# Performance work log

Measured on AMD Instinct MI355X. Metric: run time of the kernel, lower is better.

Reference implementation:

```python
import jax, jax.numpy as jnp
import numpy as np

N = 100000  # number of nodes
SELF_LOOP_W = 2.0  # improved=True in PyG GCNConv


def gcn_conv(x, edge_index, W, b):
    # x: [N, Fin], edge_index: [2, E] (row=src, col=dst), W: [Fin, Fout], b: [Fout]
    src, dst = edge_index[0], edge_index[1]
    h = x @ W  # [N, Fout]
    # degree with improved self-loops (weight 2.0)
    ones = jnp.ones(src.shape, dtype=h.dtype)
    deg = jax.ops.segment_sum(ones, dst, num_segments=N) + SELF_LOOP_W
    dinv = jnp.where(deg > 0, jax.lax.rsqrt(deg), 0.0)
    norm = dinv[src] * dinv[dst]  # [E]
    agg = jax.ops.segment_sum(h[src] * norm[:, None], dst, num_segments=N)
    # self-loop contribution: weight 2.0, norm = dinv_i * 2 * dinv_i
    agg = agg + h * (SELF_LOOP_W * dinv * dinv)[:, None]
    return agg + b


def setup_inputs() -> dict:
    key = jax.random.key(0)
    ks = jax.random.split(key, 6)
    x = jax.random.normal(ks[0], (N, 64), dtype=jnp.float32)
    edge_index = jax.random.randint(ks[1], (2, 1600000), 0, N, dtype=jnp.int64)
    W1 = jax.random.normal(ks[2], (64, 64), dtype=jnp.float32) * 0.1
    b1 = jax.random.normal(ks[3], (64,), dtype=jnp.float32) * 0.1
    W2 = jax.random.normal(ks[4], (64, 32), dtype=jnp.float32) * 0.1
    b2 = jax.random.normal(ks[5], (32,), dtype=jnp.float32) * 0.1
    return {"x": x, "edge_index": edge_index, "W1": W1, "b1": b1, "W2": W2, "b2": b2}


def reference(x, edge_index, W1, b1, W2, b2):
    h1 = jax.nn.relu(gcn_conv(x, edge_index, W1, b1))
    feature_map = h1
    out = gcn_conv(h1, edge_index, W2, b2)
    return (out, feature_map)
```

## Files before the change

kernel.cpp:

```cpp
#include <hip/hip_runtime.h>

#define N_NODES 100000
#define E_EDGES 1600000

#define BSHIFT 7
#define BSIZE 128
#define NBUCK ((N_NODES + BSIZE - 1) / BSIZE)
#define STAGE_TPB 1024
#define STAGE_EPT 16
#define STAGE_CHUNK (STAGE_TPB * STAGE_EPT)
#define NREP 4
#define BUCKET_CAP 4096

typedef __attribute__((ext_vector_type(8))) short short8;
typedef __attribute__((ext_vector_type(4))) float float4v;

__device__ inline unsigned short f2bf(float f) {
    union { float f; unsigned u; } t; t.f = f;
    unsigned r = (t.u + 0x7fffu + ((t.u >> 16) & 1u)) >> 16;
    return (unsigned short)r;
}
__device__ inline float bf2f(unsigned short h) {
    union { unsigned u; float f; } t; t.u = ((unsigned)h) << 16; return t.f;
}
__device__ inline unsigned pack_bf16x2(float a, float b) {
    return (unsigned)f2bf(a) | ((unsigned)f2bf(b) << 16);
}
__device__ inline float bf_lo(unsigned u) { union { unsigned u; float f; } t; t.u = u << 16; return t.f; }
__device__ inline float bf_hi(unsigned u) { union { unsigned u; float f; } t; t.u = u & 0xffff0000u; return t.f; }

__global__ void cursor_init_kernel(int* __restrict__ gcursor) {
    int b = blockIdx.x * blockDim.x + threadIdx.x;
    if (b < NBUCK) gcursor[b] = b * BUCKET_CAP;
}

__global__ void __launch_bounds__(STAGE_TPB) stage_kernel(
    const int* __restrict__ src, const int* __restrict__ dst,
    int* __restrict__ gcursor, unsigned* __restrict__ staged, int E) {
    __shared__ int hist[NREP][NBUCK];
    __shared__ int base[NREP][NBUCK];
    const int tid = threadIdx.x;
    const int rep = (tid >> 8) & (NREP - 1);
    const int e0 = blockIdx.x * STAGE_CHUNK;
    for (int i = tid; i < NREP * NBUCK; i += STAGE_TPB) ((int*)hist)[i] = 0;
    __syncthreads();
    int d[STAGE_EPT], s[STAGE_EPT];
#pragma unroll
    for (int k = 0; k < STAGE_EPT; ++k) {
        int e = e0 + k * STAGE_TPB + tid;
        if (e < E) {
            d[k] = dst[e];
            s[k] = src[e];
            atomicAdd(&hist[rep][d[k] >> BSHIFT], 1);
        } else {
            d[k] = -1;
        }
    }
    __syncthreads();
    for (int i = tid; i < NBUCK; i += STAGE_TPB) {
        int h0 = hist[0][i], h1 = hist[1][i], h2 = hist[2][i], h3 = hist[3][i];
        int t = h0 + h1 + h2 + h3;
        if (t > 0) {
            int g = atomicAdd(&gcursor[i], t);
            base[0][i] = g;
            base[1][i] = g + h0;
            base[2][i] = g + h0 + h1;
            base[3][i] = g + h0 + h1 + h2;
        }
    }
    __syncthreads();
#pragma unroll
    for (int k = 0; k < STAGE_EPT; ++k) {
        if (d[k] >= 0) {
            int b = d[k] >> BSHIFT;
            int pos = atomicAdd(&base[rep][b], 1);
            if (pos < (b + 1) * BUCKET_CAP)
                staged[pos] = (unsigned)s[k] | ((unsigned)(d[k] & (BSIZE - 1)) << 17);
        }
    }
}

__global__ void bscan_kernel(const int* __restrict__ gcursor, int* __restrict__ boff) {
    __shared__ int s[1024];
    const int tid = threadIdx.x;
    int v = 0;
    if (tid < NBUCK) {
        v = gcursor[tid] - tid * BUCKET_CAP;
        if (v > BUCKET_CAP) v = BUCKET_CAP;
    }
    s[tid] = v;
    __syncthreads();
    for (int off = 1; off < 1024; off <<= 1) {
        int t = (tid >= off) ? s[tid - off] : 0;
        __syncthreads();
        s[tid] += t;
        __syncthreads();
    }
    if (tid < NBUCK) boff[tid] = s[tid] - v;
    if (tid == NBUCK - 1) boff[NBUCK] = s[tid];
}

__global__ void bucket_csr_kernel(const unsigned* __restrict__ staged,
                                  const int* __restrict__ boff,
                                  int* __restrict__ deg, float* __restrict__ dinv,
                                  int* __restrict__ rowptr, int* __restrict__ csrc, int n) {
    __shared__ int ldeg[BSIZE];
    __shared__ int lrp[BSIZE];
    __shared__ int lcnt[BSIZE];
    __shared__ unsigned lrec[BUCKET_CAP];
    __shared__ int lsrc[BUCKET_CAP];
    const int b = blockIdx.x;
    const int node0 = b * BSIZE;
    const int nn = min(BSIZE, n - node0);
    const int tid = threadIdx.x;
    if (tid < BSIZE) { ldeg[tid] = 0; lcnt[tid] = 0; }
    __syncthreads();
    const int ebase = boff[b];
    const int ecnt = min(boff[b + 1] - ebase, BUCKET_CAP);
    const int sbase = b * BUCKET_CAP;
    for (int i = tid; i < ecnt; i += 256) {
        unsigned r = staged[sbase + i];
        lrec[i] = r;
        atomicAdd(&ldeg[r >> 17], 1);
    }
    __syncthreads();
    int mydeg = (tid < BSIZE) ? ldeg[tid] : 0;
    if (tid < BSIZE) lrp[tid] = mydeg;
    __syncthreads();
    for (int off = 1; off < BSIZE; off <<= 1) {
        int v = 0;
        if (tid < BSIZE && tid >= off) v = lrp[tid - off];
        __syncthreads();
        if (tid < BSIZE) lrp[tid] += v;
        __syncthreads();
    }
    if (tid < BSIZE) {
        int ex = lrp[tid] - mydeg;
        lrp[tid] = ex;
        if (tid < nn) {
            deg[node0 + tid] = mydeg;
            dinv[node0 + tid] = rsqrtf((float)mydeg + 2.0f);
            rowptr[node0 + tid] = ebase + ex;
        }
    }
    __syncthreads();
    for (int i = tid; i < ecnt; i += 256) {
        unsigned r = lrec[i];
        int dl = (int)(r >> 17);
        int sv = (int)(r & 0x1FFFFu);
        int pos = lrp[dl] + atomicAdd(&lcnt[dl], 1);
        if (pos < BUCKET_CAP) lsrc[pos] = sv;
    }
    __syncthreads();
    for (int i = tid; i < ecnt; i += 256)
        csrc[ebase + i] = lsrc[i];
}

template <int FOUT>
__global__ void __launch_bounds__(256) linear_mfma_kernel(
    const float* __restrict__ X, const float* __restrict__ W,
    const float* __restrict__ dinv, unsigned* __restrict__ HS, int n) {
    constexpr int NT = FOUT / 16;
    const int NTILES_M = n / 16;
    const int lane = threadIdx.x & 63;
    const int gwave = blockIdx.x * 4 + (threadIdx.x >> 6);
    const int nwaves = gridDim.x * 4;
    const int m = lane & 15;
    const int q = lane >> 4;

    short8 Bhi[2][NT], Blo[2][NT];
#pragma unroll
    for (int ks = 0; ks < 2; ++ks)
#pragma unroll
        for (int nt = 0; nt < NT; ++nt) {
            short8 bh, bl;
#pragma unroll
            for (int j = 0; j < 8; ++j) {
                int k = ks * 32 + q * 8 + j;
                float wv = W[k * FOUT + nt * 16 + m];
                unsigned short h = f2bf(wv);
                bh[j] = (short)h;
                bl[j] = (short)f2bf(wv - bf2f(h));
            }
            Bhi[ks][nt] = bh;
            Blo[ks][nt] = bl;
        }

    for (int tile = gwave; tile < NTILES_M; tile += nwaves) {
        const int row0 = tile * 16;
        float4v C[NT];
#pragma unroll
        for (int nt = 0; nt < NT; ++nt) C[nt] = (float4v){0.f, 0.f, 0.f, 0.f};
#pragma unroll
        for (int ks = 0; ks < 2; ++ks) {
            const float* xp = X + (size_t)(row0 + m) * 64 + ks * 32 + q * 8;
            float4v x0 = *(const float4v*)xp;
            float4v x1 = *(const float4v*)(xp + 4);
            short8 Ahi, Alo;
#pragma unroll
            for (int j = 0; j < 4; ++j) {
                unsigned short h0 = f2bf(x0[j]);
                Ahi[j] = (short)h0;
                Alo[j] = (short)f2bf(x0[j] - bf2f(h0));
                unsigned short h1 = f2bf(x1[j]);
                Ahi[4 + j] = (short)h1;
                Alo[4 + j] = (short)f2bf(x1[j] - bf2f(h1));
            }
#pragma unroll
            for (int nt = 0; nt < NT; ++nt) {
                C[nt] = __builtin_amdgcn_mfma_f32_16x16x32_bf16(Ahi, Bhi[ks][nt], C[nt], 0, 0, 0);
                C[nt] = __builtin_amdgcn_mfma_f32_16x16x32_bf16(Alo, Bhi[ks][nt], C[nt], 0, 0, 0);
                C[nt] = __builtin_amdgcn_mfma_f32_16x16x32_bf16(Ahi, Blo[ks][nt], C[nt], 0, 0, 0);
            }
        }
#pragma unroll
        for (int ch = 0; ch < NT / 2; ++ch) {
#pragma unroll
            for (int reg = 0; reg < 4; ++reg) {
                int r = row0 + q * 4 + reg;
                float di = dinv[r];
                unsigned u = pack_bf16x2(C[2 * ch][reg] * di, C[2 * ch + 1][reg] * di);
                HS[(size_t)ch * n * 16 + (size_t)r * 16 + m] = u;
            }
        }
    }
}

template <bool RELU>
__global__ void gather_chunk_kernel(const int* __restrict__ rowptr, const int* __restrict__ deg,
                                    const int* __restrict__ csrc, const unsigned* __restrict__ HS,
                                    const float* __restrict__ dinv, const float* __restrict__ bias0,
                                    float* __restrict__ OUT, int out_stride, int out_off,
                                    int n) {
    constexpr int G = 16;
    constexpr int NPB = 256 / G;
    int node = blockIdx.x * NPB + (threadIdx.x / G);
    int l = threadIdx.x % G;
    if (node >= n) return;
    int start = rowptr[node];
    int cnt = deg[node];
    unsigned us = HS[(size_t)node * G + l];
    float a0 = 2.0f * bf_lo(us);
    float a1 = 2.0f * bf_hi(us);
    float b0 = 0.0f, b1 = 0.0f;
    int j = start, end = start + cnt;
    for (; j + 7 < end; j += 8) {
        int s0 = csrc[j],     s1 = csrc[j + 1], s2 = csrc[j + 2], s3 = csrc[j + 3];
        int s4 = csrc[j + 4], s5 = csrc[j + 5], s6 = csrc[j + 6], s7 = csrc[j + 7];
        unsigned u0 = HS[(size_t)s0 * G + l];
        unsigned u1 = HS[(size_t)s1 * G + l];
        unsigned u2 = HS[(size_t)s2 * G + l];
        unsigned u3 = HS[(size_t)s3 * G + l];
        unsigned u4 = HS[(size_t)s4 * G + l];
        unsigned u5 = HS[(size_t)s5 * G + l];
        unsigned u6 = HS[(size_t)s6 * G + l];
        unsigned u7 = HS[(size_t)s7 * G + l];
        a0 += bf_lo(u0) + bf_lo(u1) + bf_lo(u2) + bf_lo(u3);
        a1 += bf_hi(u0) + bf_hi(u1) + bf_hi(u2) + bf_hi(u3);
        b0 += bf_lo(u4) + bf_lo(u5) + bf_lo(u6) + bf_lo(u7);
        b1 += bf_hi(u4) + bf_hi(u5) + bf_hi(u6) + bf_hi(u7);
    }
    for (; j + 3 < end; j += 4) {
        int s0 = csrc[j], s1 = csrc[j + 1], s2 = csrc[j + 2], s3 = csrc[j + 3];
        unsigned u0 = HS[(size_t)s0 * G + l];
        unsigned u1 = HS[(size_t)s1 * G + l];
        unsigned u2 = HS[(size_t)s2 * G + l];
        unsigned u3 = HS[(size_t)s3 * G + l];
        a0 += bf_lo(u0) + bf_lo(u1);
        a1 += bf_hi(u0) + bf_hi(u1);
        b0 += bf_lo(u2) + bf_lo(u3);
        b1 += bf_hi(u2) + bf_hi(u3);
    }
    for (; j < end; ++j) {
        unsigned u = HS[(size_t)csrc[j] * G + l];
        a0 += bf_lo(u);
        a1 += bf_hi(u);
    }
    a0 += b0;
    a1 += b1;
    float dd = dinv[node];
    float o0 = a0 * dd + bias0[l];
    float o1 = a1 * dd + bias0[16 + l];
    if (RELU) { o0 = fmaxf(o0, 0.0f); o1 = fmaxf(o1, 0.0f); }
    OUT[(size_t)node * out_stride + out_off + l] = o0;
    OUT[(size_t)node * out_stride + out_off + 16 + l] = o1;
}

extern "C" void kernel_launch(void* const* d_in, const int* in_sizes, int n_in,
                              void* d_out, int out_size, void* d_ws, size_t ws_size,
                              hipStream_t stream) {
    const float* x  = (const float*)d_in[0];
    const int*   ei = (const int*)d_in[1];
    const float* W1 = (const float*)d_in[2];
    const float* b1 = (const float*)d_in[3];
    const float* W2 = (const float*)d_in[4];
    const float* b2 = (const float*)d_in[5];

    const int* srcp = ei;
    const int* dstp = ei + E_EDGES;

    float* out = (float*)d_out;
    float* fm  = (float*)d_out + N_NODES * 32;

    char* w = (char*)d_ws;
    int*      gcursor = (int*)w;       w += sizeof(int) * NBUCK;
    int*      boff    = (int*)w;       w += sizeof(int) * (NBUCK + 1);
    int*      deg     = (int*)w;       w += sizeof(int) * N_NODES;
    int*      rowptr  = (int*)w;       w += sizeof(int) * N_NODES;
    float*    dinv    = (float*)w;     w += sizeof(float) * N_NODES;
    int*      csrc    = (int*)w;       w += sizeof(int) * E_EDGES;
    unsigned* staged  = (unsigned*)w;  w += sizeof(unsigned) * (size_t)NBUCK * BUCKET_CAP;
    unsigned* HS1     = (unsigned*)w;  w += sizeof(unsigned) * (size_t)N_NODES * 32;
    unsigned* HS2     = (unsigned*)w;  w += sizeof(unsigned) * (size_t)N_NODES * 16;

    cursor_init_kernel<<<(NBUCK + 255) / 256, 256, 0, stream>>>(gcursor);
    stage_kernel<<<(E_EDGES + STAGE_CHUNK - 1) / STAGE_CHUNK, STAGE_TPB, 0, stream>>>(
        srcp, dstp, gcursor, staged, E_EDGES);
    bscan_kernel<<<1, 1024, 0, stream>>>(gcursor, boff);
    bucket_csr_kernel<<<NBUCK, 256, 0, stream>>>(staged, boff, deg, dinv, rowptr, csrc, N_NODES);

    linear_mfma_kernel<64><<<512, 256, 0, stream>>>(x, W1, dinv, HS1, N_NODES);
    gather_chunk_kernel<true><<<(N_NODES + 15) / 16, 256, 0, stream>>>(
        rowptr, deg, csrc, HS1, dinv, b1, fm, 64, 0, N_NODES);
    gather_chunk_kernel<true><<<(N_NODES + 15) / 16, 256, 0, stream>>>(
        rowptr, deg, csrc, HS1 + (size_t)N_NODES * 16, dinv, b1 + 32, fm, 64, 32, N_NODES);

    linear_mfma_kernel<32><<<512, 256, 0, stream>>>(fm, W2, dinv, HS2, N_NODES);
    gather_chunk_kernel<false><<<(N_NODES + 15) / 16, 256, 0, stream>>>(
        rowptr, deg, csrc, HS2, dinv, b2, out, 32, 0, N_NODES);
}
```

Measured before the change: 225.1 us.

## Merge layer-1 gather launches, pack rowptr/deg into int2, shrink stage blocks

The two per-chunk gather launches for layer 1 become one launch. Adjacent blocks handle the two 32-feature chunks of the same 16 nodes, so they share the csrc and nodeinfo cache lines. Row pointer and degree are packed into one int2 array, so each node needs a single load. The staging kernel moves to 512-thread blocks with 8 edges per thread and 2 histogram replicas, which means more blocks and more global cursor atomics per bucket in exchange for less shared-memory contention per block.

Measured after the change: 219.0 us. 2.7% less time.

```diff
diff --git a/kernel.cpp b/kernel.cpp
--- a/kernel.cpp
+++ b/kernel.cpp
@@ -6,10 +6,10 @@
 #define BSHIFT 7
 #define BSIZE 128
 #define NBUCK ((N_NODES + BSIZE - 1) / BSIZE)
-#define STAGE_TPB 1024
-#define STAGE_EPT 16
+#define STAGE_TPB 512
+#define STAGE_EPT 8
 #define STAGE_CHUNK (STAGE_TPB * STAGE_EPT)
-#define NREP 4
+#define NREP 2
 #define BUCKET_CAP 4096
 
 typedef __attribute__((ext_vector_type(8))) short short8;
@@ -58,14 +58,12 @@
     }
     __syncthreads();
     for (int i = tid; i < NBUCK; i += STAGE_TPB) {
-        int h0 = hist[0][i], h1 = hist[1][i], h2 = hist[2][i], h3 = hist[3][i];
-        int t = h0 + h1 + h2 + h3;
+        int h0 = hist[0][i], h1 = hist[1][i];
+        int t = h0 + h1;
         if (t > 0) {
             int g = atomicAdd(&gcursor[i], t);
             base[0][i] = g;
             base[1][i] = g + h0;
-            base[2][i] = g + h0 + h1;
-            base[3][i] = g + h0 + h1 + h2;
         }
     }
     __syncthreads();
@@ -102,8 +100,8 @@
 
 __global__ void bucket_csr_kernel(const unsigned* __restrict__ staged,
                                   const int* __restrict__ boff,
-                                  int* __restrict__ deg, float* __restrict__ dinv,
-                                  int* __restrict__ rowptr, int* __restrict__ csrc, int n) {
+                                  int2* __restrict__ nodeinfo, float* __restrict__ dinv,
+                                  int* __restrict__ csrc, int n) {
     __shared__ int ldeg[BSIZE];
     __shared__ int lrp[BSIZE];
     __shared__ int lcnt[BSIZE];
@@ -138,9 +136,8 @@
         int ex = lrp[tid] - mydeg;
         lrp[tid] = ex;
         if (tid < nn) {
-            deg[node0 + tid] = mydeg;
+            nodeinfo[node0 + tid] = make_int2(ebase + ex, mydeg);
             dinv[node0 + tid] = rsqrtf((float)mydeg + 2.0f);
-            rowptr[node0 + tid] = ebase + ex;
         }
     }
     __syncthreads();
@@ -226,19 +223,23 @@
     }
 }
 
-template <bool RELU>
-__global__ void gather_chunk_kernel(const int* __restrict__ rowptr, const int* __restrict__ deg,
-                                    const int* __restrict__ csrc, const unsigned* __restrict__ HS,
-                                    const float* __restrict__ dinv, const float* __restrict__ bias0,
-                                    float* __restrict__ OUT, int out_stride, int out_off,
-                                    int n) {
+template <int NCHUNK, bool RELU>
+__global__ void gather_chunk_kernel(const int2* __restrict__ nodeinfo,
+                                    const int* __restrict__ csrc, const unsigned* __restrict__ HS0,
+                                    const float* __restrict__ dinv, const float* __restrict__ bias,
+                                    float* __restrict__ OUT, int n) {
     constexpr int G = 16;
     constexpr int NPB = 256 / G;
-    int node = blockIdx.x * NPB + (threadIdx.x / G);
+    const int chunk = blockIdx.x & (NCHUNK - 1);
+    int node = (blockIdx.x / NCHUNK) * NPB + (threadIdx.x / G);
     int l = threadIdx.x % G;
     if (node >= n) return;
-    int start = rowptr[node];
-    int cnt = deg[node];
+    const unsigned* __restrict__ HS = HS0 + (size_t)chunk * n * G;
+    const float* __restrict__ bias0 = bias + 32 * chunk;
+    const int out_stride = 32 * NCHUNK;
+    const int out_off = 32 * chunk;
+    int2 ni = nodeinfo[node];
+    int start = ni.x, cnt = ni.y;
     unsigned us = HS[(size_t)node * G + l];
     float a0 = 2.0f * bf_lo(us);
     float a1 = 2.0f * bf_hi(us);
@@ -303,29 +304,26 @@
     float* fm  = (float*)d_out + N_NODES * 32;
 
     char* w = (char*)d_ws;
-    int*      gcursor = (int*)w;       w += sizeof(int) * NBUCK;
-    int*      boff    = (int*)w;       w += sizeof(int) * (NBUCK + 1);
-    int*      deg     = (int*)w;       w += sizeof(int) * N_NODES;
-    int*      rowptr  = (int*)w;       w += sizeof(int) * N_NODES;
-    float*    dinv    = (float*)w;     w += sizeof(float) * N_NODES;
-    int*      csrc    = (int*)w;       w += sizeof(int) * E_EDGES;
-    unsigned* staged  = (unsigned*)w;  w += sizeof(unsigned) * (size_t)NBUCK * BUCKET_CAP;
-    unsigned* HS1     = (unsigned*)w;  w += sizeof(unsigned) * (size_t)N_NODES * 32;
-    unsigned* HS2     = (unsigned*)w;  w += sizeof(unsigned) * (size_t)N_NODES * 16;
+    int*      gcursor  = (int*)w;       w += sizeof(int) * NBUCK;
+    int*      boff     = (int*)w;       w += sizeof(int) * (NBUCK + 1);
+    int2*     nodeinfo = (int2*)w;      w += sizeof(int2) * N_NODES;
+    float*    dinv     = (float*)w;     w += sizeof(float) * N_NODES;
+    int*      csrc     = (int*)w;       w += sizeof(int) * E_EDGES;
+    unsigned* staged   = (unsigned*)w;  w += sizeof(unsigned) * (size_t)NBUCK * BUCKET_CAP;
+    unsigned* HS1      = (unsigned*)w;  w += sizeof(unsigned) * (size_t)N_NODES * 32;
+    unsigned* HS2      = (unsigned*)w;  w += sizeof(unsigned) * (size_t)N_NODES * 16;
 
     cursor_init_kernel<<<(NBUCK + 255) / 256, 256, 0, stream>>>(gcursor);
     stage_kernel<<<(E_EDGES + STAGE_CHUNK - 1) / STAGE_CHUNK, STAGE_TPB, 0, stream>>>(
         srcp, dstp, gcursor, staged, E_EDGES);
     bscan_kernel<<<1, 1024, 0, stream>>>(gcursor, boff);
-    bucket_csr_kernel<<<NBUCK, 256, 0, stream>>>(staged, boff, deg, dinv, rowptr, csrc, N_NODES);
+    bucket_csr_kernel<<<NBUCK, 256, 0, stream>>>(staged, boff, nodeinfo, dinv, csrc, N_NODES);
 
     linear_mfma_kernel<64><<<512, 256, 0, stream>>>(x, W1, dinv, HS1, N_NODES);
-    gather_chunk_kernel<true><<<(N_NODES + 15) / 16, 256, 0, stream>>>(
-        rowptr, deg, csrc, HS1, dinv, b1, fm, 64, 0, N_NODES);
-    gather_chunk_kernel<true><<<(N_NODES + 15) / 16, 256, 0, stream>>>(
-        rowptr, deg, csrc, HS1 + (size_t)N_NODES * 16, dinv, b1 + 32, fm, 64, 32, N_NODES);
+    gather_chunk_kernel<2, true><<<2 * ((N_NODES + 15) / 16), 256, 0, stream>>>(
+        nodeinfo, csrc, HS1, dinv, b1, fm, N_NODES);
 
     linear_mfma_kernel<32><<<512, 256, 0, stream>>>(fm, W2, dinv, HS2, N_NODES);
-    gather_chunk_kernel<false><<<(N_NODES + 15) / 16, 256, 0, stream>>>(
-        rowptr, deg, csrc, HS2, dinv, b2, out, 32, 0, N_NODES);
-}
+    gather_chunk_kernel<1, false><<<(N_NODES + 15) / 16, 256, 0, stream>>>(
+        nodeinfo, csrc, HS2, dinv, b2, out, N_NODES);
+}
```
